# Kernel optimization log

Measured on AMD Instinct MI355X. Metric: run time of the kernel, lower is better.

## Reference

```python
import jax, jax.numpy as jnp
import numpy as np
from jax import lax

B, N, NPOINT, NSAMPLE = 4, 8192, 2048, 32
IN_CH = 64
MLP = (64, 64, 128)
RADIUS = 0.2
BN_EPS = 1e-5
BIG = 1e10


def _fps(xyz, npoint):
    # Farthest point sampling; deterministic start at index 0 (torch uses random start).
    b, n, _ = xyz.shape

    def body(carry, _):
        dist, far = carry
        cen = jnp.take_along_axis(xyz, far[:, None, None], axis=1)  # (B,1,3)
        d = jnp.sum((xyz - cen) ** 2, axis=-1)                      # (B,N)
        dist = jnp.minimum(dist, d)
        return (dist, jnp.argmax(dist, axis=-1).astype(jnp.int32)), far

    init = (jnp.full((b, n), BIG, xyz.dtype), jnp.zeros((b,), jnp.int32))
    _, cents = lax.scan(body, init, None, length=npoint)            # (npoint,B)
    return jnp.transpose(cents)                                     # (B,npoint)


def _sqdist(src, dst):
    # |src|^2 + |dst|^2 - 2 src.dst, clamped at 0 (matches square_distance)
    d = (jnp.sum(src ** 2, -1, keepdims=True)
         + jnp.sum(dst ** 2, -1, keepdims=True).swapaxes(1, 2)
         - 2.0 * jnp.einsum('bsc,bnc->bsn', src, dst))
    return jnp.maximum(d, 0.0)


def _ball_query(radius, nsample, xyz, new_xyz):
    sq = _sqdist(new_xyz, xyz)                           # (B,S,N)
    masked = jnp.where(sq > radius ** 2, BIG, sq)
    _, gidx = lax.top_k(-masked, nsample)                # nsample smallest dists
    gath = jnp.take_along_axis(sq, gidx, axis=2)
    # replace out-of-radius neighbors with the closest (first) neighbor
    return jnp.where(gath > radius ** 2, gidx[:, :, :1], gidx)


def _gather(points, idx):
    # points (B,N,C), idx (B,...) -> (B,...,C)
    return jax.vmap(lambda p, i: p[i])(points, idx)


def _forward(xyz, features, layers):
    fps_idx = _fps(xyz, NPOINT)                          # (B,S)
    new_xyz = _gather(xyz, fps_idx)                      # (B,S,3)
    idx = _ball_query(RADIUS, NSAMPLE, xyz, new_xyz)     # (B,S,K)
    g_xyz = _gather(xyz, idx) - new_xyz[:, :, None, :]   # (B,S,K,3) centered
    g_feat = _gather(features, idx)                      # (B,S,K,C)
    h = jnp.concatenate([g_xyz, g_feat], axis=-1)        # (B,S,K,3+C)
    for (W, g, b, m, v) in layers:                       # conv1x1 + BN(eval) + ReLU
        h = jnp.einsum('bskc,oc->bsko', h, W)
        h = jax.nn.relu((h - m) / jnp.sqrt(v + BN_EPS) * g + b)
    return new_xyz, jnp.max(h, axis=2)                   # max over neighbors K


def setup_inputs() -> dict:
    key = jax.random.key(0)
    ks = jax.random.split(key, 20)
    inp = {
        'xyz': jax.random.uniform(ks[0], (B, N, 3), jnp.float32),
        'features': jax.random.normal(ks[1], (B, N, IN_CH), jnp.float32),
    }
    last = IN_CH + 3
    k = 2
    for i, out in enumerate(MLP):
        inp[f'W{i}'] = jax.random.normal(ks[k], (out, last), jnp.float32) / np.sqrt(last); k += 1
        inp[f'gamma{i}'] = jax.random.uniform(ks[k], (out,), jnp.float32, 0.5, 1.5); k += 1
        inp[f'beta{i}'] = 0.1 * jax.random.normal(ks[k], (out,), jnp.float32); k += 1
        inp[f'mean{i}'] = 0.1 * jax.random.normal(ks[k], (out,), jnp.float32); k += 1
        inp[f'var{i}'] = jax.random.uniform(ks[k], (out,), jnp.float32, 0.5, 1.5); k += 1
        last = out
    return inp


def reference(xyz, features, W0, gamma0, beta0, mean0, var0, W1, gamma1, beta1, mean1, var1, W2, gamma2, beta2, mean2, var2):
    layers = [(W0, gamma0, beta0, mean0, var0),
              (W1, gamma1, beta1, mean1, var1),
              (W2, gamma2, beta2, mean2, var2)]
    return _forward(xyz, features, layers)
```

## Files before the change

kernel.cpp:

```cpp
#include <hip/hip_runtime.h>
#include <cstdint>

#define NPTS 8192
#define NBATCH 4
#define NS 2048
#define NK 32
#define CIN 64
#define C0 67
#define H1 64
#define H2 64
#define H3 128
#define CAP 1024
#define BIGF 1e10f

#define WT0_OFF 0
#define B0_OFF  4288
#define WT1_OFF 4352
#define B1_OFF  8448
#define WT2_OFF 8512
#define B2_OFF  16704
#define FPS_OFF 16832

__device__ __forceinline__ float sq3(float ax, float ay, float az) {
  return __fadd_rn(__fadd_rn(__fmul_rn(ax, ax), __fmul_rn(ay, ay)), __fmul_rn(az, az));
}

#define PAIRRED(dv, iv, ctrl)                                                          \
  {                                                                                    \
    int _sd = __builtin_amdgcn_update_dpp(__float_as_int(dv), __float_as_int(dv),      \
                                          (ctrl), 0xf, 0xf, false);                    \
    int _si = __builtin_amdgcn_update_dpp((iv), (iv), (ctrl), 0xf, 0xf, false);        \
    float _fd = __int_as_float(_sd);                                                   \
    bool _tk = (_fd > (dv)) || ((_fd == (dv)) && (_si < (iv)));                        \
    (dv) = _tk ? _fd : (dv);                                                           \
    (iv) = _tk ? _si : (iv);                                                           \
  }

__global__ void fold_kernel(const float* __restrict__ W0, const float* __restrict__ g0, const float* __restrict__ be0, const float* __restrict__ m0, const float* __restrict__ v0,
                            const float* __restrict__ W1, const float* __restrict__ g1, const float* __restrict__ be1, const float* __restrict__ m1, const float* __restrict__ v1,
                            const float* __restrict__ W2, const float* __restrict__ g2, const float* __restrict__ be2, const float* __restrict__ m2, const float* __restrict__ v2,
                            float* __restrict__ ws) {
  int t = blockIdx.x * 256 + threadIdx.x;
  if (t < C0 * H1) {
    int c = t / H1, o = t - c * H1;
    float sc = g0[o] / sqrtf(v0[o] + 1e-5f);
    ws[WT0_OFF + t] = W0[o * C0 + c] * sc;
  } else if (t < B0_OFF + H1) {
    int o = t - B0_OFF;
    float sc = g0[o] / sqrtf(v0[o] + 1e-5f);
    ws[t] = be0[o] - m0[o] * sc;
  } else if (t < WT1_OFF + H1 * H2) {
    int t2 = t - WT1_OFF; int c = t2 / H2, o = t2 - c * H2;
    float sc = g1[o] / sqrtf(v1[o] + 1e-5f);
    ws[t] = W1[o * H1 + c] * sc;
  } else if (t < B1_OFF + H2) {
    int o = t - B1_OFF;
    float sc = g1[o] / sqrtf(v1[o] + 1e-5f);
    ws[t] = be1[o] - m1[o] * sc;
  } else if (t < WT2_OFF + H2 * H3) {
    int t2 = t - WT2_OFF; int c = t2 / H3, o = t2 - c * H3;
    float sc = g2[o] / sqrtf(v2[o] + 1e-5f);
    ws[t] = W2[o * H2 + c] * sc;
  } else if (t < B2_OFF + H3) {
    int o = t - B2_OFF;
    float sc = g2[o] / sqrtf(v2[o] + 1e-5f);
    ws[t] = be2[o] - m2[o] * sc;
  }
}

__global__ __launch_bounds__(256, 1)
void fps_kernel(const float* __restrict__ xyz, float* __restrict__ newxyz, int* __restrict__ fpsidx) {
  const int b = blockIdx.x;
  const float* px = xyz + (size_t)b * NPTS * 3;
  const int tid = threadIdx.x;
  const int lane = tid & 63;
  const int wv = tid >> 6;

  float X[32], Y[32], Z[32], D[32];
#pragma unroll
  for (int j = 0; j < 32; ++j) {
    int p = tid * 32 + j;
    X[j] = px[p * 3 + 0];
    Y[j] = px[p * 3 + 1];
    Z[j] = px[p * 3 + 2];
    D[j] = BIGF;
  }

  __shared__ float cndD[2][4];
  __shared__ int cndI[2][4];
  __shared__ float oX[NS], oY[NS], oZ[NS];
  __shared__ int oI[NS];

  float cx = px[0], cy = px[1], cz = px[2];
  if (tid == 0) { oI[0] = 0; oX[0] = cx; oY[0] = cy; oZ[0] = cz; }

  int par = 0;
  for (int t = 1; t < NS; ++t) {
    float bd = -1.0f; int bi = 0;
#pragma unroll
    for (int j = 0; j < 32; ++j) {
      float dx = __fsub_rn(X[j], cx);
      float dy = __fsub_rn(Y[j], cy);
      float dz = __fsub_rn(Z[j], cz);
      float d = sq3(dx, dy, dz);
      float nd = fminf(D[j], d);
      D[j] = nd;
      bool gt = nd > bd;
      bd = gt ? nd : bd;
      bi = gt ? (tid * 32 + j) : bi;
    }
    PAIRRED(bd, bi, 0x121);
    PAIRRED(bd, bi, 0x122);
    PAIRRED(bd, bi, 0x124);
    PAIRRED(bd, bi, 0x128);
    PAIRRED(bd, bi, 0x142);
    PAIRRED(bd, bi, 0x143);
    if (lane == 63) { cndD[par][wv] = bd; cndI[par][wv] = bi; }
    __syncthreads();

    const int ci = lane & 3;
    float pd = cndD[par][ci];
    int pi = cndI[par][ci];
    PAIRRED(pd, pi, 0x121);
    PAIRRED(pd, pi, 0x122);
    const int far = __builtin_amdgcn_readfirstlane(pi);
    const float* pc = px + 3 * (size_t)far;
    cx = pc[0]; cy = pc[1]; cz = pc[2];
    if (tid == 0) { oI[t] = far; oX[t] = cx; oY[t] = cy; oZ[t] = cz; }
    par ^= 1;
  }
  __syncthreads();

  for (int i = tid; i < NS; i += 256) {
    fpsidx[b * NS + i] = oI[i];
    float* o = newxyz + ((size_t)b * NS + i) * 3;
    o[0] = oX[i]; o[1] = oY[i]; o[2] = oZ[i];
  }
}

__global__ __launch_bounds__(256)
void sa_kernel(const float* __restrict__ xyz, const float* __restrict__ feat,
               const float* __restrict__ ws, const int* __restrict__ fpsidx,
               const float* __restrict__ newxyz, float* __restrict__ outf) {
  const int bs = blockIdx.x;
  const int b = bs >> 11;
  const int s = bs & (NS - 1);
  const int tid = threadIdx.x;
  const int lane = tid & 63;

  __shared__ __align__(16) unsigned long long cand[CAP];
  __shared__ int cntS;
  __shared__ int sel[NK];
  __shared__ float hA[32 * 69];
  __shared__ float hB[32 * 65];

  const float* px = xyz + (size_t)b * NPTS * 3;
  const float* pf = feat + (size_t)b * NPTS * CIN;
  const size_t srow = (size_t)b * NS + s;
  const float cx = newxyz[srow * 3 + 0];
  const float cy = newxyz[srow * 3 + 1];
  const float cz = newxyz[srow * 3 + 2];

  if (tid == 0) cntS = 0;
  __syncthreads();

  const float ssrc = sq3(cx, cy, cz);
  const float R2F = 0.04f;
  for (int p = tid; p < NPTS; p += 256) {
    float x = px[p * 3 + 0], y = px[p * 3 + 1], z = px[p * 3 + 2];
    float sdst = sq3(x, y, z);
    float dot = __fadd_rn(__fadd_rn(__fmul_rn(cx, x), __fmul_rn(cy, y)), __fmul_rn(cz, z));
    float d = __fsub_rn(__fadd_rn(ssrc, sdst), __fmul_rn(2.0f, dot));
    d = fmaxf(d, 0.0f);
    bool hit = (d <= R2F);
    unsigned long long m = __ballot(hit);
    if (m) {
      int base = 0;
      if (lane == 0) base = atomicAdd(&cntS, __popcll(m));
      base = __shfl(base, 0);
      if (hit) {
        int pos = base + __popcll(m & ((1ull << lane) - 1ull));
        if (pos < CAP)
          cand[pos] = ((unsigned long long)__float_as_uint(d) << 32) | (unsigned long long)(unsigned)p;
      }
    }
  }
  __syncthreads();

  {
    const int cnt = min(cntS, CAP);
    if (cnt <= 256) {
      unsigned long long k0 = (tid < cnt) ? cand[tid] : ~0ull;
      int r0 = 0;
      int j = 0;
      for (; j + 2 <= cnt; j += 2) {
        ulonglong2 kj = *(const ulonglong2*)&cand[j];
        r0 += (kj.x < k0) ? 1 : 0;
        r0 += (kj.y < k0) ? 1 : 0;
      }
      if (j < cnt) r0 += (cand[j] < k0) ? 1 : 0;
      if (tid < cnt) {
        if (r0 < NK) sel[r0] = (int)(k0 & 0xffffffffull);
        if (r0 == 0) {
          for (int q = cnt; q < NK; ++q) sel[q] = (int)(k0 & 0xffffffffull);
        }
      }
    } else if (cnt <= 512) {
      unsigned long long k0 = cand[tid];
      unsigned long long k1 = (256 + tid < cnt) ? cand[256 + tid] : ~0ull;
      int r0 = 0, r1 = 0;
      int j = 0;
      for (; j + 2 <= cnt; j += 2) {
        ulonglong2 kj = *(const ulonglong2*)&cand[j];
        r0 += (kj.x < k0) ? 1 : 0; r0 += (kj.y < k0) ? 1 : 0;
        r1 += (kj.x < k1) ? 1 : 0; r1 += (kj.y < k1) ? 1 : 0;
      }
      if (j < cnt) { unsigned long long kj = cand[j]; r0 += (kj < k0) ? 1 : 0; r1 += (kj < k1) ? 1 : 0; }
      if (r0 < NK) sel[r0] = (int)(k0 & 0xffffffffull);
      if (256 + tid < cnt && r1 < NK) sel[r1] = (int)(k1 & 0xffffffffull);
    } else {
      unsigned long long k0 = cand[tid];
      unsigned long long k1 = cand[256 + tid];
      unsigned long long k2 = (512 + tid < cnt) ? cand[512 + tid] : ~0ull;
      unsigned long long k3 = (768 + tid < cnt) ? cand[768 + tid] : ~0ull;
      int r0 = 0, r1 = 0, r2 = 0, r3 = 0;
      int j = 0;
      for (; j + 2 <= cnt; j += 2) {
        ulonglong2 kj = *(const ulonglong2*)&cand[j];
        r0 += (kj.x < k0) ? 1 : 0; r0 += (kj.y < k0) ? 1 : 0;
        r1 += (kj.x < k1) ? 1 : 0; r1 += (kj.y < k1) ? 1 : 0;
        r2 += (kj.x < k2) ? 1 : 0; r2 += (kj.y < k2) ? 1 : 0;
        r3 += (kj.x < k3) ? 1 : 0; r3 += (kj.y < k3) ? 1 : 0;
      }
      if (j < cnt) {
        unsigned long long kj = cand[j];
        r0 += (kj < k0) ? 1 : 0; r1 += (kj < k1) ? 1 : 0;
        r2 += (kj < k2) ? 1 : 0; r3 += (kj < k3) ? 1 : 0;
      }
      if (r0 < NK) sel[r0] = (int)(k0 & 0xffffffffull);
      if (r1 < NK) sel[r1] = (int)(k1 & 0xffffffffull);
      if (512 + tid < cnt && r2 < NK) sel[r2] = (int)(k2 & 0xffffffffull);
      if (768 + tid < cnt && r3 < NK) sel[r3] = (int)(k3 & 0xffffffffull);
    }
  }
  __syncthreads();

  {
    int kk = tid >> 3, j = tid & 7;
    int ip = sel[kk];
    const float* fr = pf + (size_t)ip * CIN + j * 8;
    float4 a = *(const float4*)(fr);
    float4 c4 = *(const float4*)(fr + 4);
    float* hrow = hA + kk * 69 + 3 + j * 8;
    hrow[0] = a.x;  hrow[1] = a.y;  hrow[2] = a.z;  hrow[3] = a.w;
    hrow[4] = c4.x; hrow[5] = c4.y; hrow[6] = c4.z; hrow[7] = c4.w;
  }
  if (tid < 32) {
    int ip = sel[tid];
    hA[tid * 69 + 0] = px[ip * 3 + 0] - cx;
    hA[tid * 69 + 1] = px[ip * 3 + 1] - cy;
    hA[tid * 69 + 2] = px[ip * 3 + 2] - cz;
  }
  __syncthreads();

  const int k = tid & 31;
  const int ob = tid >> 5;

  {
    const float* Wt = ws + WT0_OFF;
    const float* bb = ws + B0_OFF;
    const int o0 = ob * 8;
    float acc[8];
#pragma unroll
    for (int i = 0; i < 8; ++i) acc[i] = bb[o0 + i];
    const float* hrow = hA + k * 69;
    for (int c = 0; c < C0; ++c) {
      float h = hrow[c];
      const float4 w0 = *(const float4*)(Wt + c * H1 + o0);
      const float4 w1 = *(const float4*)(Wt + c * H1 + o0 + 4);
      acc[0] = fmaf(h, w0.x, acc[0]); acc[1] = fmaf(h, w0.y, acc[1]);
      acc[2] = fmaf(h, w0.z, acc[2]); acc[3] = fmaf(h, w0.w, acc[3]);
      acc[4] = fmaf(h, w1.x, acc[4]); acc[5] = fmaf(h, w1.y, acc[5]);
      acc[6] = fmaf(h, w1.z, acc[6]); acc[7] = fmaf(h, w1.w, acc[7]);
    }
    float* orow = hB + k * 65 + o0;
#pragma unroll
    for (int i = 0; i < 8; ++i) orow[i] = fmaxf(acc[i], 0.0f);
  }
  __syncthreads();

  {
    const float* Wt = ws + WT1_OFF;
    const float* bb = ws + B1_OFF;
    const int o0 = ob * 8;
    float acc[8];
#pragma unroll
    for (int i = 0; i < 8; ++i) acc[i] = bb[o0 + i];
    const float* hrow = hB + k * 65;
    for (int c = 0; c < H1; ++c) {
      float h = hrow[c];
      const float4 w0 = *(const float4*)(Wt + c * H2 + o0);
      const float4 w1 = *(const float4*)(Wt + c * H2 + o0 + 4);
      acc[0] = fmaf(h, w0.x, acc[0]); acc[1] = fmaf(h, w0.y, acc[1]);
      acc[2] = fmaf(h, w0.z, acc[2]); acc[3] = fmaf(h, w0.w, acc[3]);
      acc[4] = fmaf(h, w1.x, acc[4]); acc[5] = fmaf(h, w1.y, acc[5]);
      acc[6] = fmaf(h, w1.z, acc[6]); acc[7] = fmaf(h, w1.w, acc[7]);
    }
    float* orow = hA + k * 65 + o0;
#pragma unroll
    for (int i = 0; i < 8; ++i) orow[i] = fmaxf(acc[i], 0.0f);
  }
  __syncthreads();

  {
    const float* Wt = ws + WT2_OFF;
    const float* bb = ws + B2_OFF;
    const int o0 = ob * 16;
    float acc[16];
#pragma unroll
    for (int i = 0; i < 16; ++i) acc[i] = bb[o0 + i];
    const float* hrow = hA + k * 65;
    for (int c = 0; c < H2; ++c) {
      float h = hrow[c];
      const float4 w0 = *(const float4*)(Wt + c * H3 + o0);
      const float4 w1 = *(const float4*)(Wt + c * H3 + o0 + 4);
      const float4 w2 = *(const float4*)(Wt + c * H3 + o0 + 8);
      const float4 w3 = *(const float4*)(Wt + c * H3 + o0 + 12);
      acc[0]  = fmaf(h, w0.x, acc[0]);  acc[1]  = fmaf(h, w0.y, acc[1]);
      acc[2]  = fmaf(h, w0.z, acc[2]);  acc[3]  = fmaf(h, w0.w, acc[3]);
      acc[4]  = fmaf(h, w1.x, acc[4]);  acc[5]  = fmaf(h, w1.y, acc[5]);
      acc[6]  = fmaf(h, w1.z, acc[6]);  acc[7]  = fmaf(h, w1.w, acc[7]);
      acc[8]  = fmaf(h, w2.x, acc[8]);  acc[9]  = fmaf(h, w2.y, acc[9]);
      acc[10] = fmaf(h, w2.z, acc[10]); acc[11] = fmaf(h, w2.w, acc[11]);
      acc[12] = fmaf(h, w3.x, acc[12]); acc[13] = fmaf(h, w3.y, acc[13]);
      acc[14] = fmaf(h, w3.z, acc[14]); acc[15] = fmaf(h, w3.w, acc[15]);
    }
#pragma unroll
    for (int i = 0; i < 16; ++i) acc[i] = fmaxf(acc[i], 0.0f);
#pragma unroll
    for (int m = 1; m < 32; m <<= 1) {
#pragma unroll
      for (int i = 0; i < 16; ++i) {
        float o = __shfl_xor(acc[i], m);
        acc[i] = fmaxf(acc[i], o);
      }
    }
    if (k == 0) {
      float* op = outf + srow * H3 + o0;
      *(float4*)(op + 0)  = make_float4(acc[0],  acc[1],  acc[2],  acc[3]);
      *(float4*)(op + 4)  = make_float4(acc[4],  acc[5],  acc[6],  acc[7]);
      *(float4*)(op + 8)  = make_float4(acc[8],  acc[9],  acc[10], acc[11]);
      *(float4*)(op + 12) = make_float4(acc[12], acc[13], acc[14], acc[15]);
    }
  }
}

extern "C" void kernel_launch(void* const* d_in, const int* in_sizes, int n_in,
                              void* d_out, int out_size, void* d_ws, size_t ws_size,
                              hipStream_t stream) {
  const float* xyz  = (const float*)d_in[0];
  const float* feat = (const float*)d_in[1];
  const float* W0 = (const float*)d_in[2];
  const float* g0 = (const float*)d_in[3];
  const float* be0 = (const float*)d_in[4];
  const float* m0 = (const float*)d_in[5];
  const float* v0 = (const float*)d_in[6];
  const float* W1 = (const float*)d_in[7];
  const float* g1 = (const float*)d_in[8];
  const float* be1 = (const float*)d_in[9];
  const float* m1 = (const float*)d_in[10];
  const float* v1 = (const float*)d_in[11];
  const float* W2 = (const float*)d_in[12];
  const float* g2 = (const float*)d_in[13];
  const float* be2 = (const float*)d_in[14];
  const float* m2 = (const float*)d_in[15];
  const float* v2 = (const float*)d_in[16];

  float* out = (float*)d_out;
  float* ws = (float*)d_ws;
  int* fpsidx = (int*)(ws + FPS_OFF);
  float* outfeat = out + (size_t)NBATCH * NS * 3;

  fold_kernel<<<(B2_OFF + H3 + 255) / 256, 256, 0, stream>>>(
      W0, g0, be0, m0, v0, W1, g1, be1, m1, v1, W2, g2, be2, m2, v2, ws);
  fps_kernel<<<NBATCH, 256, 0, stream>>>(xyz, out, fpsidx);
  sa_kernel<<<NBATCH * NS, 256, 0, stream>>>(xyz, feat, ws, fpsidx, out, outfeat);
}
```

Before: 2.867 ms.

## Pack FPS distance math into v_pk f32 ops and stage point coordinates in LDS

The farthest-point-sampling loop now computes squared distances two points at a time with packed v_pk_add/v_pk_mul f32 instructions. The coordinates of the selected centroid are read from an LDS copy of all points rather than from global memory, which removes a global load latency from every serial iteration. The candidate distance and index for each wave are packed into one shared 8-byte slot, and results are written straight to global memory. The cost is 128KB of LDS and inline asm that could block compiler scheduling. Rounding stays in the same order as before, so results should be unchanged.

```diff
diff --git a/kernel.cpp b/kernel.cpp
--- a/kernel.cpp
+++ b/kernel.cpp
@@ -21,8 +21,26 @@
 #define B2_OFF  16704
 #define FPS_OFF 16832
 
+typedef float f32x2 __attribute__((ext_vector_type(2)));
+
 __device__ __forceinline__ float sq3(float ax, float ay, float az) {
   return __fadd_rn(__fadd_rn(__fmul_rn(ax, ax), __fmul_rn(ay, ay)), __fmul_rn(az, az));
+}
+
+__device__ __forceinline__ f32x2 pk_sub(f32x2 a, f32x2 b) {
+  f32x2 r;
+  asm("v_pk_add_f32 %0, %1, %2 neg_lo:[0,1] neg_hi:[0,1]" : "=v"(r) : "v"(a), "v"(b));
+  return r;
+}
+__device__ __forceinline__ f32x2 pk_mul(f32x2 a, f32x2 b) {
+  f32x2 r;
+  asm("v_pk_mul_f32 %0, %1, %2" : "=v"(r) : "v"(a), "v"(b));
+  return r;
+}
+__device__ __forceinline__ f32x2 pk_add(f32x2 a, f32x2 b) {
+  f32x2 r;
+  asm("v_pk_add_f32 %0, %1, %2" : "=v"(r) : "v"(a), "v"(b));
+  return r;
 }
 
 #define PAIRRED(dv, iv, ctrl)                                                          \
@@ -76,38 +94,57 @@
   const int lane = tid & 63;
   const int wv = tid >> 6;
 
-  float X[32], Y[32], Z[32], D[32];
-#pragma unroll
-  for (int j = 0; j < 32; ++j) {
-    int p = tid * 32 + j;
-    X[j] = px[p * 3 + 0];
-    Y[j] = px[p * 3 + 1];
-    Z[j] = px[p * 3 + 2];
-    D[j] = BIGF;
-  }
-
-  __shared__ float cndD[2][4];
-  __shared__ int cndI[2][4];
-  __shared__ float oX[NS], oY[NS], oZ[NS];
-  __shared__ int oI[NS];
+  __shared__ __align__(16) float lco[NPTS * 4];
+  __shared__ __align__(8) float cnd[2][4][2];
+
+  f32x2 X2[16], Y2[16], Z2[16], D2[16];
+#pragma unroll
+  for (int jj = 0; jj < 16; ++jj) {
+    int p0 = tid * 32 + 2 * jj;
+    float x0 = px[p0 * 3 + 0], y0 = px[p0 * 3 + 1], z0 = px[p0 * 3 + 2];
+    float x1 = px[p0 * 3 + 3], y1 = px[p0 * 3 + 4], z1 = px[p0 * 3 + 5];
+    X2[jj][0] = x0; X2[jj][1] = x1;
+    Y2[jj][0] = y0; Y2[jj][1] = y1;
+    Z2[jj][0] = z0; Z2[jj][1] = z1;
+    D2[jj][0] = BIGF; D2[jj][1] = BIGF;
+    *(float4*)&lco[(size_t)p0 * 4]       = make_float4(x0, y0, z0, 0.0f);
+    *(float4*)&lco[(size_t)(p0 + 1) * 4] = make_float4(x1, y1, z1, 0.0f);
+  }
 
   float cx = px[0], cy = px[1], cz = px[2];
-  if (tid == 0) { oI[0] = 0; oX[0] = cx; oY[0] = cy; oZ[0] = cz; }
+  if (tid == 0) {
+    fpsidx[b * NS] = 0;
+    float* o = newxyz + (size_t)b * NS * 3;
+    o[0] = cx; o[1] = cy; o[2] = cz;
+  }
+  __syncthreads();
 
   int par = 0;
   for (int t = 1; t < NS; ++t) {
+    f32x2 cpx, cpy, cpz;
+    cpx[0] = cx; cpx[1] = cx;
+    cpy[0] = cy; cpy[1] = cy;
+    cpz[0] = cz; cpz[1] = cz;
     float bd = -1.0f; int bi = 0;
 #pragma unroll
-    for (int j = 0; j < 32; ++j) {
-      float dx = __fsub_rn(X[j], cx);
-      float dy = __fsub_rn(Y[j], cy);
-      float dz = __fsub_rn(Z[j], cz);
-      float d = sq3(dx, dy, dz);
-      float nd = fminf(D[j], d);
-      D[j] = nd;
-      bool gt = nd > bd;
-      bd = gt ? nd : bd;
-      bi = gt ? (tid * 32 + j) : bi;
+    for (int jj = 0; jj < 16; ++jj) {
+      f32x2 dx = pk_sub(X2[jj], cpx);
+      f32x2 dy = pk_sub(Y2[jj], cpy);
+      f32x2 dz = pk_sub(Z2[jj], cpz);
+      f32x2 xx = pk_mul(dx, dx);
+      f32x2 yy = pk_mul(dy, dy);
+      f32x2 ss = pk_add(xx, yy);
+      f32x2 zz = pk_mul(dz, dz);
+      f32x2 dd = pk_add(ss, zz);
+      float n0 = fminf(D2[jj][0], dd[0]);
+      float n1 = fminf(D2[jj][1], dd[1]);
+      D2[jj][0] = n0; D2[jj][1] = n1;
+      bool g0 = n0 > bd;
+      bd = g0 ? n0 : bd;
+      bi = g0 ? (tid * 32 + 2 * jj) : bi;
+      bool g1 = n1 > bd;
+      bd = g1 ? n1 : bd;
+      bi = g1 ? (tid * 32 + 2 * jj + 1) : bi;
     }
     PAIRRED(bd, bi, 0x121);
     PAIRRED(bd, bi, 0x122);
@@ -115,26 +152,27 @@
     PAIRRED(bd, bi, 0x128);
     PAIRRED(bd, bi, 0x142);
     PAIRRED(bd, bi, 0x143);
-    if (lane == 63) { cndD[par][wv] = bd; cndI[par][wv] = bi; }
+    if (lane == 63) {
+      cnd[par][wv][0] = bd;
+      cnd[par][wv][1] = __int_as_float(bi);
+    }
     __syncthreads();
 
     const int ci = lane & 3;
-    float pd = cndD[par][ci];
-    int pi = cndI[par][ci];
+    f32x2 cc = *(const f32x2*)&cnd[par][ci][0];
+    float pd = cc[0];
+    int pi = __float_as_int(cc[1]);
     PAIRRED(pd, pi, 0x121);
     PAIRRED(pd, pi, 0x122);
     const int far = __builtin_amdgcn_readfirstlane(pi);
-    const float* pc = px + 3 * (size_t)far;
-    cx = pc[0]; cy = pc[1]; cz = pc[2];
-    if (tid == 0) { oI[t] = far; oX[t] = cx; oY[t] = cy; oZ[t] = cz; }
+    float4 c4 = *(const float4*)&lco[(size_t)far * 4];
+    cx = c4.x; cy = c4.y; cz = c4.z;
+    if (tid == 0) {
+      fpsidx[b * NS + t] = far;
+      float* o = newxyz + ((size_t)b * NS + t) * 3;
+      o[0] = cx; o[1] = cy; o[2] = cz;
+    }
     par ^= 1;
-  }
-  __syncthreads();
-
-  for (int i = tid; i < NS; i += 256) {
-    fpsidx[b * NS + i] = oI[i];
-    float* o = newxyz + ((size_t)b * NS + i) * 3;
-    o[0] = oX[i]; o[1] = oY[i]; o[2] = oZ[i];
   }
 }
 
```

Measured after the change: 2.691 ms. -6.1%, faster.
